# Performance work log

Measured on AMD Instinct MI355X. Metric: run time of the kernel, lower is better.

Reference implementation:

```python
import jax, jax.numpy as jnp
import numpy as np

B, K, D, H, L = 128, 128, 768, 8, 4
HD = D // H
FF = 4 * D
SIM = D // 4
BOOST = 0.3
SCALE = HD ** -0.5
EPS = 1e-5


def _ln(x, g, b):
    m = x.mean(-1, keepdims=True)
    v = ((x - m) ** 2).mean(-1, keepdims=True)
    return (x - m) * jax.lax.rsqrt(v + EPS) * g + b


def setup_inputs() -> dict:
    key = jax.random.key(0)
    ks = jax.random.split(key, 10)
    def n(k, shape, s=0.02):
        return jax.random.normal(k, shape, dtype=jnp.float32) * s
    return {
        'slots': jax.random.normal(ks[0], (B, K, D), dtype=jnp.float32),
        'pos_emb': n(ks[1], (1, K, D)),
        'Wq': n(ks[2], (L, D, D)),
        'Wk': n(ks[3], (L, D, D)),
        'Wv': n(ks[4], (L, D, D)),
        'Wo': n(ks[5], (L, D, D)),
        'bo': jnp.zeros((L, D), jnp.float32),
        'Wsim': n(ks[6], (L, D, SIM)),
        'g1': jnp.ones((L, D), jnp.float32),
        'b1': jnp.zeros((L, D), jnp.float32),
        'g2': jnp.ones((L, D), jnp.float32),
        'b2': jnp.zeros((L, D), jnp.float32),
        'Wff1': n(ks[7], (L, D, FF)),
        'bff1': jnp.zeros((L, FF), jnp.float32),
        'Wff2': n(ks[8], (L, FF, D)),
        'bff2': jnp.zeros((L, D), jnp.float32),
        'gf': jnp.ones((D,), jnp.float32),
        'bf': jnp.zeros((D,), jnp.float32),
    }


def reference(slots, pos_emb, Wq, Wk, Wv, Wo, bo, Wsim, g1, b1, g2, b2,
              Wff1, bff1, Wff2, bff2, gf, bf):
    x = slots + pos_emb  # K == max_slots -> full pos table
    for l in range(L):
        # --- similarity-biased multi-head self-attention (pre-norm) ---
        nx = _ln(x, g1[l], b1[l])
        q = (nx @ Wq[l]).reshape(B, K, H, HD)
        k = (nx @ Wk[l]).reshape(B, K, H, HD)
        v = (nx @ Wv[l]).reshape(B, K, H, HD)
        scores = jnp.einsum('bqhd,bkhd->bhqk', q, k) * SCALE  # [B,H,K,K]
        s = nx @ Wsim[l]  # [B,K,D/4]
        s = s / jnp.maximum(jnp.linalg.norm(s, axis=-1, keepdims=True), 1e-12)
        sim = jnp.einsum('bqc,bkc->bqk', s, s)  # cosine similarity matrix
        scores = scores + BOOST * sim[:, None, :, :]
        a = jax.nn.softmax(scores, axis=-1)
        o = jnp.einsum('bhqk,bkhd->bqhd', a, v).reshape(B, K, D)
        x = x + (o @ Wo[l] + bo[l])
        # --- feed-forward (pre-norm) ---
        nx = _ln(x, g2[l], b2[l])
        h = jax.nn.gelu(nx @ Wff1[l] + bff1[l], approximate=False)
        x = x + (h @ Wff2[l] + bff2[l])
    return _ln(x, gf, bf)
```

## Files before the change

### kernel.cpp

```cpp
#include <hip/hip_runtime.h>

typedef unsigned short u16;
typedef unsigned int u32;
typedef float f32x4 __attribute__((ext_vector_type(4)));
typedef __bf16 bf16x8 __attribute__((ext_vector_type(8)));

static constexpr int D = 768, FFD = 3072, SIMC = 192, NH = 8, HD = 96;
static constexpr int B = 128, K = 128, M = B * K, NL = 4;
static constexpr int QKVW = 2560;
static constexpr int SIMOFF = 2304;
static constexpr float QSCALE = 0.14724502f;
static constexpr float SBOOST2 = 0.6578821f;
static constexpr float EPS_F = 1e-5f;

__device__ __forceinline__ float bf2f(u16 u) {
  union { u32 i; float f; } v; v.i = ((u32)u) << 16; return v.f;
}
__device__ __forceinline__ u16 f2bf(float f) {
  union { float f; u32 i; } v; v.f = f;
  u32 u = v.i;
  u32 r = (u + 0x7FFFu + ((u >> 16) & 1u)) >> 16;
  return (u16)r;
}

__device__ __forceinline__ float fast_gelu(float x) {
  float u2 = x * (2.3020585f + 0.102944f * x * x);
  float e = __builtin_amdgcn_exp2f(u2);
  float r = __builtin_amdgcn_rcpf(1.0f + e);
  return x - x * r;
}

__device__ __forceinline__ void gload16(const void* g, void* l) {
  __builtin_amdgcn_global_load_lds(
      (const __attribute__((address_space(1))) void*)g,
      (__attribute__((address_space(3))) void*)l, 16, 0, 0);
}

__global__ __launch_bounds__(256) void addpos_kernel(
    const float* __restrict__ slots, const float* __restrict__ pos,
    u16* __restrict__ x) {
  int i = blockIdx.x * 256 + threadIdx.x;
  int m = i / D;
  int d = i - m * D;
  x[i] = f2bf(slots[i] + pos[(m & (K - 1)) * D + d]);
}

__device__ __forceinline__ float block_sum(float v, float* sbuf) {
#pragma unroll
  for (int off = 32; off > 0; off >>= 1) v += __shfl_xor(v, off, 64);
  int lane = threadIdx.x & 63, w = threadIdx.x >> 6;
  if (lane == 0) sbuf[w] = v;
  __syncthreads();
  v = sbuf[0] + sbuf[1] + sbuf[2] + sbuf[3];
  __syncthreads();
  return v;
}

template <bool OUT_BF16>
__global__ __launch_bounds__(256) void ln_kernel(
    const u16* __restrict__ x, const float* __restrict__ g,
    const float* __restrict__ b, void* __restrict__ out) {
  __shared__ float sbuf[4];
  int row = blockIdx.x, tid = threadIdx.x;
  const u16* xr = x + (size_t)row * D;
  float v0 = bf2f(xr[tid]), v1 = bf2f(xr[tid + 256]), v2 = bf2f(xr[tid + 512]);
  float s = block_sum(v0 + v1 + v2, sbuf);
  float mean = s * (1.0f / D);
  float d0 = v0 - mean, d1 = v1 - mean, d2 = v2 - mean;
  float sq = block_sum(d0 * d0 + d1 * d1 + d2 * d2, sbuf);
  float rs = rsqrtf(sq * (1.0f / D) + EPS_F);
  float y0 = d0 * rs * g[tid] + b[tid];
  float y1 = d1 * rs * g[tid + 256] + b[tid + 256];
  float y2 = d2 * rs * g[tid + 512] + b[tid + 512];
  if (OUT_BF16) {
    u16* o = (u16*)out + (size_t)row * D;
    o[tid] = f2bf(y0); o[tid + 256] = f2bf(y1); o[tid + 512] = f2bf(y2);
  } else {
    float* o = (float*)out + (size_t)row * D;
    o[tid] = y0; o[tid + 256] = y1; o[tid + 512] = y2;
  }
}

struct W4 {
  const float* w0; const float* w1; const float* w2; const float* w3;
  u16* o0; u16* o1; u16* o2; u16* o3;
};
__global__ __launch_bounds__(256) void wconv4_kernel(W4 p, float scale0) {
  __shared__ u16 t[32][33];
  int z = blockIdx.z;
  const float* W = z == 0 ? p.w0 : z == 1 ? p.w1 : z == 2 ? p.w2 : p.w3;
  u16* Wt = z == 0 ? p.o0 : z == 1 ? p.o1 : z == 2 ? p.o2 : p.o3;
  float sc = z == 0 ? scale0 : 1.0f;
  int n0 = blockIdx.x * 32, k0 = blockIdx.y * 32;
  int tid = threadIdx.x;
  int c = tid & 31, r4 = tid >> 5;
#pragma unroll
  for (int i = 0; i < 4; ++i) {
    int r = r4 + i * 8;
    t[r][c] = f2bf(W[(size_t)(k0 + r) * D + n0 + c] * sc);
  }
  __syncthreads();
#pragma unroll
  for (int i = 0; i < 4; ++i) {
    int r = r4 + i * 8;
    Wt[(size_t)(n0 + r) * D + k0 + c] = t[c][r];
  }
}

__global__ __launch_bounds__(256) void wconv_kernel(
    const float* __restrict__ W, u16* __restrict__ Wt, int N, int Kd) {
  __shared__ u16 t[32][33];
  int n0 = blockIdx.x * 32, k0 = blockIdx.y * 32;
  int tid = threadIdx.x;
  int c = tid & 31, r4 = tid >> 5;
#pragma unroll
  for (int i = 0; i < 4; ++i) {
    int r = r4 + i * 8;
    t[r][c] = f2bf(W[(size_t)(k0 + r) * N + n0 + c]);
  }
  __syncthreads();
#pragma unroll
  for (int i = 0; i < 4; ++i) {
    int r = r4 + i * 8;
    Wt[(size_t)(n0 + r) * Kd + k0 + c] = t[c][r];
  }
}

template <bool OUT_BF16, bool BIAS, bool GELU_, bool RESID>
__global__ __launch_bounds__(512, 2) void gemm256_kernel(
    const u16* __restrict__ A, const u16* __restrict__ Bt,
    const float* __restrict__ bias, const u16* __restrict__ resid,
    void* __restrict__ Cout, int N, int Kdim, int NBX) {
  __shared__ u16 lds[65536];
  int tid = threadIdx.x;
  int w = tid >> 6, lane = tid & 63;
  int wm = w >> 2, wn = w & 3;
  int lr = lane & 15, lg = lane >> 4;

  int nwg = gridDim.x;
  int cpx = nwg >> 3;
  int swz = (blockIdx.x & 7) * cpx + (blockIdx.x >> 3);
  int bx = swz % NBX, by = swz / NBX;
  int n0 = bx << 8, m0 = by << 8;

  int scol = ((lane & 7) ^ (lane >> 3)) << 3;
  size_t aOff = (size_t)((w << 4) + (lane >> 3)) * Kdim + scol;
  u16* ldsU = lds;

  auto stageA = [&](int buf, int h, int t) {
    const u16* g = A + (size_t)(m0 + (h << 7)) * Kdim + ((size_t)t << 6) + aOff;
    u16* l = ldsU + buf * 32768 + h * 8192 + (w << 10);
    gload16(g, l);
    gload16(g + ((size_t)Kdim << 3), l + 512);
  };
  auto stageB = [&](int buf, int h, int t) {
    const u16* g = Bt + (size_t)(n0 + (h << 7)) * Kdim + ((size_t)t << 6) + aOff;
    u16* l = ldsU + buf * 32768 + 16384 + h * 8192 + (w << 10);
    gload16(g, l);
    gload16(g + ((size_t)Kdim << 3), l + 512);
  };

  const u16* lA0p = ldsU;
  const u16* lB0p = ldsU + 16384;
  const u16* lA1p = ldsU + 32768;
  const u16* lB1p = ldsU + 49152;
  int arow = (wm * 128 + lr) * 64;
  int brow = (wn * 64 + lr) * 64;
  int swz0 = (((lg * 16)) ^ ((lr & 7) << 4)) >> 1;
  int swz1 = ((64 + lg * 16) ^ ((lr & 7) << 4)) >> 1;

  f32x4 acc[8][4] = {};
  bf16x8 ar[2][4], br[2][4];

#define READ_A(BASE, MSEG)                                                   \
  do {                                                                       \
    _Pragma("unroll") for (int mm = 0; mm < 4; ++mm) {                       \
      const u16* p_ = (BASE) + arow + ((MSEG) * 64 + mm * 16) * 64;          \
      ar[0][mm] = *(const bf16x8*)(p_ + swz0);                               \
      ar[1][mm] = *(const bf16x8*)(p_ + swz1);                               \
    }                                                                        \
  } while (0)
#define READ_B(BASE, NSEG)                                                   \
  do {                                                                       \
    _Pragma("unroll") for (int nn = 0; nn < 2; ++nn) {                       \
      const u16* p_ = (BASE) + brow + ((NSEG) * 32 + nn * 16) * 64;          \
      br[0][(NSEG) * 2 + nn] = *(const bf16x8*)(p_ + swz0);                  \
      br[1][(NSEG) * 2 + nn] = *(const bf16x8*)(p_ + swz1);                  \
    }                                                                        \
  } while (0)
#define MFMA_Q(MSEG, NSEG)                                                   \
  do {                                                                       \
    __builtin_amdgcn_s_setprio(1);                                           \
    _Pragma("unroll") for (int ks = 0; ks < 2; ++ks)                         \
      _Pragma("unroll") for (int mm = 0; mm < 4; ++mm)                       \
        _Pragma("unroll") for (int nn = 0; nn < 2; ++nn)                     \
          acc[(MSEG) * 4 + mm][(NSEG) * 2 + nn] =                            \
              __builtin_amdgcn_mfma_f32_16x16x32_bf16(                       \
                  ar[ks][mm], br[ks][(NSEG) * 2 + nn],                       \
                  acc[(MSEG) * 4 + mm][(NSEG) * 2 + nn], 0, 0, 0);           \
    __builtin_amdgcn_s_setprio(0);                                           \
  } while (0)
#define PSYNC()                                                              \
  do {                                                                       \
    __builtin_amdgcn_sched_barrier(0);                                       \
    asm volatile("s_waitcnt lgkmcnt(0)" ::: "memory");                       \
    __builtin_amdgcn_s_barrier();                                            \
    __builtin_amdgcn_sched_barrier(0);                                       \
  } while (0)
#define PSYNC_V(N)                                                           \
  do {                                                                       \
    __builtin_amdgcn_sched_barrier(0);                                       \
    asm volatile("s_waitcnt vmcnt(" #N ") lgkmcnt(0)" ::: "memory");         \
    __builtin_amdgcn_s_barrier();                                            \
    __builtin_amdgcn_sched_barrier(0);                                       \
  } while (0)

  int NK = Kdim >> 6, NI = NK >> 1;
  stageA(0, 0, 0); stageA(0, 1, 0); stageB(0, 0, 0); stageB(0, 1, 0);
  stageB(1, 0, 1); stageB(1, 1, 1);
  asm volatile("s_waitcnt vmcnt(4)" ::: "memory");
  __builtin_amdgcn_s_barrier();
  __builtin_amdgcn_sched_barrier(0);

  for (int i = 0; i < NI; ++i) {
    int t1 = 2 * i + 1, t2 = 2 * i + 2, t3 = 2 * i + 3;
    bool last = (i == NI - 1);
    READ_A(lA0p, 0); READ_B(lB0p, 0);
    stageA(1, 0, t1);
    PSYNC(); MFMA_Q(0, 0);
    READ_B(lB0p, 1);
    stageA(1, 1, t1);
    PSYNC(); MFMA_Q(0, 1);
    READ_A(lA0p, 1);
    if (!last) stageB(0, 0, t2);
    PSYNC(); MFMA_Q(1, 0);
    if (!last) { stageB(0, 1, t2); PSYNC_V(4); }
    else PSYNC_V(0);
    MFMA_Q(1, 1);
    READ_A(lA1p, 0); READ_B(lB1p, 0);
    if (!last) stageA(0, 0, t2);
    PSYNC(); MFMA_Q(0, 0);
    READ_B(lB1p, 1);
    if (!last) stageA(0, 1, t2);
    PSYNC(); MFMA_Q(0, 1);
    READ_A(lA1p, 1);
    if (!last) stageB(1, 0, t3);
    PSYNC(); MFMA_Q(1, 0);
    if (!last) { stageB(1, 1, t3); PSYNC_V(4); }
    else PSYNC();
    MFMA_Q(1, 1);
  }

#pragma unroll
  for (int m = 0; m < 8; ++m) {
#pragma unroll
    for (int n = 0; n < 4; ++n) {
      int col = n0 + wn * 64 + n * 16 + lr;
      float bv = BIAS ? bias[col] : 0.0f;
#pragma unroll
      for (int r = 0; r < 4; ++r) {
        int row = m0 + wm * 128 + m * 16 + lg * 4 + r;
        float v = acc[m][n][r];
        if (BIAS) v += bv;
        if (GELU_) v = fast_gelu(v);
        if (RESID) v += bf2f(resid[(size_t)row * N + col]);
        if (OUT_BF16) ((u16*)Cout)[(size_t)row * N + col] = f2bf(v);
        else ((float*)Cout)[(size_t)row * N + col] = v;
      }
    }
  }
#undef READ_A
#undef READ_B
#undef MFMA_Q
#undef PSYNC
#undef PSYNC_V
}

__global__ __launch_bounds__(64) void snorm_kernel(
    const u16* __restrict__ qkvb, u16* __restrict__ sbf) {
  int row = blockIdx.x, lane = threadIdx.x;
  const u16* sr = qkvb + (size_t)row * QKVW + SIMOFF;
  float v0 = bf2f(sr[lane]), v1 = bf2f(sr[lane + 64]), v2 = bf2f(sr[lane + 128]);
  float sq = v0 * v0 + v1 * v1 + v2 * v2;
#pragma unroll
  for (int off = 32; off > 0; off >>= 1) sq += __shfl_xor(sq, off, 64);
  float inv = SBOOST2 / fmaxf(sqrtf(sq), 1e-12f);
  u16* o = sbf + (size_t)row * SIMC;
  o[lane] = f2bf(v0 * inv);
  o[lane + 64] = f2bf(v1 * inv);
  o[lane + 128] = f2bf(v2 * inv);
}

__global__ __launch_bounds__(256) void attn_kernel(
    const u16* __restrict__ qkv, const u16* __restrict__ sbf,
    u16* __restrict__ ob) {
  __shared__ u16 Vt[96][136];
  __shared__ u16 Pl[4][32][136];
  int bh = blockIdx.x, b = bh >> 3, h = bh & 7;
  int tid = threadIdx.x, w = tid >> 6, lane = tid & 63;
  int lr = lane & 15, lg = lane >> 4;
  const u16* qb = qkv + (size_t)b * K * QKVW + h * HD;
  const u16* kb = qb + D;
  const u16* vb = qb + 2 * D;
  const u16* sb = sbf + (size_t)b * K * SIMC;
  for (int idx = tid; idx < 128 * 12; idx += 256) {
    int r = idx / 12, db = idx - r * 12;
    uint4 v4 = *(const uint4*)(vb + (size_t)r * QKVW + db * 8);
    u32 vv[4] = {v4.x, v4.y, v4.z, v4.w};
#pragma unroll
    for (int j = 0; j < 4; ++j) {
      Vt[db * 8 + 2 * j][r] = (u16)(vv[j] & 0xffffu);
      Vt[db * 8 + 2 * j + 1][r] = (u16)(vv[j] >> 16);
    }
  }
  int q0 = 32 * w;
  f32x4 accs[2][8] = {};
#pragma unroll
  for (int ks = 0; ks < 3; ++ks) {
    bf16x8 af[2];
#pragma unroll
    for (int m = 0; m < 2; ++m)
      af[m] = *(const bf16x8*)(qb + (size_t)(q0 + 16 * m + lr) * QKVW + ks * 32 + lg * 8);
#pragma unroll
    for (int n = 0; n < 8; ++n) {
      bf16x8 bf = *(const bf16x8*)(kb + (size_t)(16 * n + lr) * QKVW + ks * 32 + lg * 8);
#pragma unroll
      for (int m = 0; m < 2; ++m)
        accs[m][n] = __builtin_amdgcn_mfma_f32_16x16x32_bf16(af[m], bf, accs[m][n], 0, 0, 0);
    }
  }
#pragma unroll
  for (int ks = 0; ks < 6; ++ks) {
    bf16x8 af[2];
#pragma unroll
    for (int m = 0; m < 2; ++m)
      af[m] = *(const bf16x8*)(sb + (size_t)(q0 + 16 * m + lr) * SIMC + ks * 32 + lg * 8);
#pragma unroll
    for (int n = 0; n < 8; ++n) {
      bf16x8 bf = *(const bf16x8*)(sb + (size_t)(16 * n + lr) * SIMC + ks * 32 + lg * 8);
#pragma unroll
      for (int m = 0; m < 2; ++m)
        accs[m][n] = __builtin_amdgcn_mfma_f32_16x16x32_bf16(af[m], bf, accs[m][n], 0, 0, 0);
    }
  }
#pragma unroll
  for (int m = 0; m < 2; ++m) {
    float mx[4] = {-3e38f, -3e38f, -3e38f, -3e38f};
#pragma unroll
    for (int n = 0; n < 8; ++n)
#pragma unroll
      for (int r = 0; r < 4; ++r) mx[r] = fmaxf(mx[r], accs[m][n][r]);
#pragma unroll
    for (int r = 0; r < 4; ++r) {
      mx[r] = fmaxf(mx[r], __shfl_xor(mx[r], 1, 64));
      mx[r] = fmaxf(mx[r], __shfl_xor(mx[r], 2, 64));
      mx[r] = fmaxf(mx[r], __shfl_xor(mx[r], 4, 64));
      mx[r] = fmaxf(mx[r], __shfl_xor(mx[r], 8, 64));
    }
    float sm[4] = {0.f, 0.f, 0.f, 0.f};
#pragma unroll
    for (int n = 0; n < 8; ++n)
#pragma unroll
      for (int r = 0; r < 4; ++r) {
        float e = __builtin_amdgcn_exp2f(accs[m][n][r] - mx[r]);
        accs[m][n][r] = e;
        sm[r] += e;
      }
#pragma unroll
    for (int r = 0; r < 4; ++r) {
      sm[r] += __shfl_xor(sm[r], 1, 64);
      sm[r] += __shfl_xor(sm[r], 2, 64);
      sm[r] += __shfl_xor(sm[r], 4, 64);
      sm[r] += __shfl_xor(sm[r], 8, 64);
    }
    float inv[4];
#pragma unroll
    for (int r = 0; r < 4; ++r) inv[r] = 1.0f / sm[r];
#pragma unroll
    for (int n = 0; n < 8; ++n)
#pragma unroll
      for (int r = 0; r < 4; ++r)
        Pl[w][16 * m + 4 * lg + r][16 * n + lr] = f2bf(accs[m][n][r] * inv[r]);
  }
  __syncthreads();
  f32x4 acco[2][6] = {};
#pragma unroll
  for (int ks = 0; ks < 4; ++ks) {
    bf16x8 pa[2];
#pragma unroll
    for (int m = 0; m < 2; ++m)
      pa[m] = *(const bf16x8*)(&Pl[w][16 * m + lr][ks * 32 + lg * 8]);
#pragma unroll
    for (int n = 0; n < 6; ++n) {
      bf16x8 bv = *(const bf16x8*)(&Vt[16 * n + lr][ks * 32 + lg * 8]);
#pragma unroll
      for (int m = 0; m < 2; ++m)
        acco[m][n] = __builtin_amdgcn_mfma_f32_16x16x32_bf16(pa[m], bv, acco[m][n], 0, 0, 0);
    }
  }
  u16* obb = ob + (size_t)b * K * D + h * HD;
#pragma unroll
  for (int m = 0; m < 2; ++m)
#pragma unroll
    for (int n = 0; n < 6; ++n)
#pragma unroll
      for (int r = 0; r < 4; ++r)
        obb[(size_t)(q0 + 16 * m + 4 * lg + r) * D + 16 * n + lr] = f2bf(acco[m][n][r]);
}

extern "C" void kernel_launch(void* const* d_in, const int* in_sizes, int n_in,
                              void* d_out, int out_size, void* d_ws, size_t ws_size,
                              hipStream_t stream) {
  (void)in_sizes; (void)n_in; (void)out_size;
  const float* slots = (const float*)d_in[0];
  const float* pos   = (const float*)d_in[1];
  const float* Wq    = (const float*)d_in[2];
  const float* Wk    = (const float*)d_in[3];
  const float* Wv    = (const float*)d_in[4];
  const float* Wo    = (const float*)d_in[5];
  const float* bo    = (const float*)d_in[6];
  const float* Wsim  = (const float*)d_in[7];
  const float* g1    = (const float*)d_in[8];
  const float* b1    = (const float*)d_in[9];
  const float* g2    = (const float*)d_in[10];
  const float* b2    = (const float*)d_in[11];
  const float* Wff1  = (const float*)d_in[12];
  const float* bff1  = (const float*)d_in[13];
  const float* Wff2  = (const float*)d_in[14];
  const float* bff2  = (const float*)d_in[15];
  const float* gf    = (const float*)d_in[16];
  const float* bfin  = (const float*)d_in[17];

  char* p = (char*)d_ws;
  u16*   x    = (u16*)p;   p += (size_t)M * D * 2;
  u16*   nx   = (u16*)p;   p += (size_t)M * D * 2;
  u16*   qkvb = (u16*)p;   p += (size_t)M * QKVW * 2;
  u16*   ob   = (u16*)p;   p += (size_t)M * D * 2;
  u16*   sbf  = (u16*)p;   p += (size_t)M * SIMC * 2;
  u16*   wtA  = (u16*)p;   p += (size_t)QKVW * D * 2;
  u16*   wtB  = (u16*)p;   p += (size_t)D * D * 2;
  u16*   wtC  = (u16*)p;   p += (size_t)FFD * D * 2;
  u16*   wtD  = (u16*)p;   p += (size_t)D * FFD * 2;
  if ((size_t)(p - (char*)d_ws) > ws_size) return;
  u16* hb = qkvb;

  hipMemsetAsync(wtA + (size_t)(SIMOFF + SIMC) * D, 0, (size_t)64 * D * 2, stream);

  addpos_kernel<<<M * D / 256, 256, 0, stream>>>(slots, pos, x);

  dim3 gw4(24, 24, 4);
  dim3 gwsim(SIMC / 32, 24);
  dim3 gw1(96, 24);
  dim3 gw2(24, 96);
  int nbx_qkv = QKVW / 256, nwg_qkv = nbx_qkv * (M / 256);
  int nbx_o   = D / 256,    nwg_o   = nbx_o * (M / 256);
  int nbx_f1  = FFD / 256,  nwg_f1  = nbx_f1 * (M / 256);

  for (int l = 0; l < NL; ++l) {
    ln_kernel<true><<<M, 256, 0, stream>>>(x, g1 + l * D, b1 + l * D, nx);
    W4 wp = {Wq + (size_t)l * D * D, Wk + (size_t)l * D * D,
             Wv + (size_t)l * D * D, Wo + (size_t)l * D * D,
             wtA, wtA + D * D, wtA + 2 * D * D, wtB};
    wconv4_kernel<<<gw4, 256, 0, stream>>>(wp, QSCALE);
    wconv_kernel<<<gwsim, 256, 0, stream>>>(Wsim + (size_t)l * D * SIMC,
                                            wtA + (size_t)SIMOFF * D, SIMC, D);
    wconv_kernel<<<gw1, 256, 0, stream>>>(Wff1 + (size_t)l * D * FFD, wtC, FFD, D);
    wconv_kernel<<<gw2, 256, 0, stream>>>(Wff2 + (size_t)l * FFD * D, wtD, D, FFD);
    gemm256_kernel<true, false, false, false><<<nwg_qkv, 512, 0, stream>>>(
        nx, wtA, nullptr, nullptr, qkvb, QKVW, D, nbx_qkv);
    snorm_kernel<<<M, 64, 0, stream>>>(qkvb, sbf);
    attn_kernel<<<B * NH, 256, 0, stream>>>(qkvb, sbf, ob);
    gemm256_kernel<true, true, false, true><<<nwg_o, 512, 0, stream>>>(
        ob, wtB, bo + l * D, x, x, D, D, nbx_o);
    ln_kernel<true><<<M, 256, 0, stream>>>(x, g2 + l * D, b2 + l * D, nx);
    gemm256_kernel<true, true, true, false><<<nwg_f1, 512, 0, stream>>>(
        nx, wtC, bff1 + l * FFD, nullptr, hb, FFD, D, nbx_f1);
    gemm256_kernel<true, true, false, true><<<nwg_o, 512, 0, stream>>>(
        hb, wtD, bff2 + l * D, x, x, D, FFD, nbx_o);
  }
  ln_kernel<false><<<M, 256, 0, stream>>>(x, gf, bfin, d_out);
}
```

Baseline: 1.524 ms.

## Reorder GEMM main loop LDS reads/syncs and merge weight conversion kernels

The GEMM inner loop is reordered so each quadrant issues its global staging and both k-halves of LDS fragment reads before its MFMAs, with the barrier placed after the MFMAs rather than before. This is meant to overlap LDS latency and barriers with matrix math. Separately, the four per-layer weight transpose/convert launches are merged into one flat-indexed kernel to cut launch overhead. The barrier reordering risks hazards between LDS reads and the next stage writes, and the larger fragment-register live ranges could raise register pressure.

Result: no change. 1.508 ms (-1.1%).

```diff
diff --git a/kernel.cpp b/kernel.cpp
--- a/kernel.cpp
+++ b/kernel.cpp
@@ -81,42 +81,42 @@
   }
 }
 
-struct W4 {
-  const float* w0; const float* w1; const float* w2; const float* w3;
-  u16* o0; u16* o1; u16* o2; u16* o3;
+struct WAll {
+  const float *wq, *wk, *wv, *wo, *wsim, *wff1, *wff2;
+  u16 *tA, *tB, *tC, *tD;
 };
-__global__ __launch_bounds__(256) void wconv4_kernel(W4 p, float scale0) {
+__global__ __launch_bounds__(256) void wconv_all_kernel(WAll p, float qscale) {
   __shared__ u16 t[32][33];
-  int z = blockIdx.z;
-  const float* W = z == 0 ? p.w0 : z == 1 ? p.w1 : z == 2 ? p.w2 : p.w3;
-  u16* Wt = z == 0 ? p.o0 : z == 1 ? p.o1 : z == 2 ? p.o2 : p.o3;
-  float sc = z == 0 ? scale0 : 1.0f;
-  int n0 = blockIdx.x * 32, k0 = blockIdx.y * 32;
+  int bid = blockIdx.x;
+  const float* W; u16* Wt; int N, Kd, n0, k0;
+  float sc = 1.0f;
+  if (bid < 2304) {
+    int z = bid / 576, rem = bid - z * 576;
+    W = z == 0 ? p.wq : z == 1 ? p.wk : z == 2 ? p.wv : p.wo;
+    Wt = z == 0 ? p.tA : z == 1 ? p.tA + 768 * 768
+       : z == 2 ? p.tA + 2 * 768 * 768 : p.tB;
+    if (z == 0) sc = qscale;
+    N = 768; Kd = 768;
+    n0 = (rem % 24) * 32; k0 = (rem / 24) * 32;
+  } else if (bid < 2448) {
+    int rem = bid - 2304;
+    W = p.wsim; Wt = p.tA + (size_t)SIMOFF * 768; N = SIMC; Kd = 768;
+    n0 = (rem % 6) * 32; k0 = (rem / 6) * 32;
+  } else if (bid < 4752) {
+    int rem = bid - 2448;
+    W = p.wff1; Wt = p.tC; N = FFD; Kd = 768;
+    n0 = (rem % 96) * 32; k0 = (rem / 96) * 32;
+  } else {
+    int rem = bid - 4752;
+    W = p.wff2; Wt = p.tD; N = 768; Kd = FFD;
+    n0 = (rem % 24) * 32; k0 = (rem / 24) * 32;
+  }
   int tid = threadIdx.x;
   int c = tid & 31, r4 = tid >> 5;
 #pragma unroll
   for (int i = 0; i < 4; ++i) {
     int r = r4 + i * 8;
-    t[r][c] = f2bf(W[(size_t)(k0 + r) * D + n0 + c] * sc);
-  }
-  __syncthreads();
-#pragma unroll
-  for (int i = 0; i < 4; ++i) {
-    int r = r4 + i * 8;
-    Wt[(size_t)(n0 + r) * D + k0 + c] = t[c][r];
-  }
-}
-
-__global__ __launch_bounds__(256) void wconv_kernel(
-    const float* __restrict__ W, u16* __restrict__ Wt, int N, int Kd) {
-  __shared__ u16 t[32][33];
-  int n0 = blockIdx.x * 32, k0 = blockIdx.y * 32;
-  int tid = threadIdx.x;
-  int c = tid & 31, r4 = tid >> 5;
-#pragma unroll
-  for (int i = 0; i < 4; ++i) {
-    int r = r4 + i * 8;
-    t[r][c] = f2bf(W[(size_t)(k0 + r) * N + n0 + c]);
+    t[r][c] = f2bf(W[(size_t)(k0 + r) * N + n0 + c] * sc);
   }
   __syncthreads();
 #pragma unroll
@@ -172,20 +172,18 @@
   f32x4 acc[8][4] = {};
   bf16x8 ar[2][4], br[2][4];
 
-#define READ_A(BASE, MSEG)                                                   \
+#define READ_A_KS(BASE, MSEG, KS)                                            \
   do {                                                                       \
     _Pragma("unroll") for (int mm = 0; mm < 4; ++mm) {                       \
       const u16* p_ = (BASE) + arow + ((MSEG) * 64 + mm * 16) * 64;          \
-      ar[0][mm] = *(const bf16x8*)(p_ + swz0);                               \
-      ar[1][mm] = *(const bf16x8*)(p_ + swz1);                               \
+      ar[KS][mm] = *(const bf16x8*)(p_ + ((KS) ? swz1 : swz0));              \
     }                                                                        \
   } while (0)
-#define READ_B(BASE, NSEG)                                                   \
+#define READ_B_KS(BASE, NSEG, KS)                                            \
   do {                                                                       \
     _Pragma("unroll") for (int nn = 0; nn < 2; ++nn) {                       \
       const u16* p_ = (BASE) + brow + ((NSEG) * 32 + nn * 16) * 64;          \
-      br[0][(NSEG) * 2 + nn] = *(const bf16x8*)(p_ + swz0);                  \
-      br[1][(NSEG) * 2 + nn] = *(const bf16x8*)(p_ + swz1);                  \
+      br[KS][(NSEG) * 2 + nn] = *(const bf16x8*)(p_ + ((KS) ? swz1 : swz0)); \
     }                                                                        \
   } while (0)
 #define MFMA_Q(MSEG, NSEG)                                                   \
@@ -225,30 +223,40 @@
   for (int i = 0; i < NI; ++i) {
     int t1 = 2 * i + 1, t2 = 2 * i + 2, t3 = 2 * i + 3;
     bool last = (i == NI - 1);
-    READ_A(lA0p, 0); READ_B(lB0p, 0);
     stageA(1, 0, t1);
-    PSYNC(); MFMA_Q(0, 0);
-    READ_B(lB0p, 1);
+    READ_A_KS(lA0p, 0, 0); READ_B_KS(lB0p, 0, 0);
+    READ_A_KS(lA0p, 0, 1); READ_B_KS(lB0p, 0, 1);
+    MFMA_Q(0, 0);
+    PSYNC();
     stageA(1, 1, t1);
-    PSYNC(); MFMA_Q(0, 1);
-    READ_A(lA0p, 1);
+    READ_B_KS(lB0p, 1, 0); READ_B_KS(lB0p, 1, 1);
+    MFMA_Q(0, 1);
+    PSYNC();
     if (!last) stageB(0, 0, t2);
-    PSYNC(); MFMA_Q(1, 0);
-    if (!last) { stageB(0, 1, t2); PSYNC_V(4); }
-    else PSYNC_V(0);
+    READ_A_KS(lA0p, 1, 0); READ_A_KS(lA0p, 1, 1);
+    MFMA_Q(1, 0);
+    PSYNC();
+    if (!last) stageB(0, 1, t2);
     MFMA_Q(1, 1);
-    READ_A(lA1p, 0); READ_B(lB1p, 0);
+    if (last) PSYNC_V(0);
+    else      PSYNC_V(4);
     if (!last) stageA(0, 0, t2);
-    PSYNC(); MFMA_Q(0, 0);
-    READ_B(lB1p, 1);
+    READ_A_KS(lA1p, 0, 0); READ_B_KS(lB1p, 0, 0);
+    READ_A_KS(lA1p, 0, 1); READ_B_KS(lB1p, 0, 1);
+    MFMA_Q(0, 0);
+    PSYNC();
     if (!last) stageA(0, 1, t2);
-    PSYNC(); MFMA_Q(0, 1);
-    READ_A(lA1p, 1);
+    READ_B_KS(lB1p, 1, 0); READ_B_KS(lB1p, 1, 1);
+    MFMA_Q(0, 1);
+    PSYNC();
     if (!last) stageB(1, 0, t3);
-    PSYNC(); MFMA_Q(1, 0);
-    if (!last) { stageB(1, 1, t3); PSYNC_V(4); }
-    else PSYNC();
+    READ_A_KS(lA1p, 1, 0); READ_A_KS(lA1p, 1, 1);
+    MFMA_Q(1, 0);
+    PSYNC();
+    if (!last) stageB(1, 1, t3);
     MFMA_Q(1, 1);
+    if (last) PSYNC();
+    else      PSYNC_V(4);
   }
 
 #pragma unroll
@@ -269,8 +277,8 @@
       }
     }
   }
-#undef READ_A
-#undef READ_B
+#undef READ_A_KS
+#undef READ_B_KS
 #undef MFMA_Q
 #undef PSYNC
 #undef PSYNC_V
@@ -448,24 +456,18 @@
 
   addpos_kernel<<<M * D / 256, 256, 0, stream>>>(slots, pos, x);
 
-  dim3 gw4(24, 24, 4);
-  dim3 gwsim(SIMC / 32, 24);
-  dim3 gw1(96, 24);
-  dim3 gw2(24, 96);
   int nbx_qkv = QKVW / 256, nwg_qkv = nbx_qkv * (M / 256);
   int nbx_o   = D / 256,    nwg_o   = nbx_o * (M / 256);
   int nbx_f1  = FFD / 256,  nwg_f1  = nbx_f1 * (M / 256);
 
   for (int l = 0; l < NL; ++l) {
     ln_kernel<true><<<M, 256, 0, stream>>>(x, g1 + l * D, b1 + l * D, nx);
-    W4 wp = {Wq + (size_t)l * D * D, Wk + (size_t)l * D * D,
-             Wv + (size_t)l * D * D, Wo + (size_t)l * D * D,
-             wtA, wtA + D * D, wtA + 2 * D * D, wtB};
-    wconv4_kernel<<<gw4, 256, 0, stream>>>(wp, QSCALE);
-    wconv_kernel<<<gwsim, 256, 0, stream>>>(Wsim + (size_t)l * D * SIMC,
-                                            wtA + (size_t)SIMOFF * D, SIMC, D);
-    wconv_kernel<<<gw1, 256, 0, stream>>>(Wff1 + (size_t)l * D * FFD, wtC, FFD, D);
-    wconv_kernel<<<gw2, 256, 0, stream>>>(Wff2 + (size_t)l * FFD * D, wtD, D, FFD);
+    WAll wp = {Wq + (size_t)l * D * D, Wk + (size_t)l * D * D,
+               Wv + (size_t)l * D * D, Wo + (size_t)l * D * D,
+               Wsim + (size_t)l * D * SIMC,
+               Wff1 + (size_t)l * D * FFD, Wff2 + (size_t)l * FFD * D,
+               wtA, wtB, wtC, wtD};
+    wconv_all_kernel<<<7056, 256, 0, stream>>>(wp, QSCALE);
     gemm256_kernel<true, false, false, false><<<nwg_qkv, 512, 0, stream>>>(
         nx, wtA, nullptr, nullptr, qkvb, QKVW, D, nbx_qkv);
     snorm_kernel<<<M, 64, 0, stream>>>(qkvb, sbf);
```
